# Optimization experiments

Measured on AMD Instinct MI355X. Metric: run time of the kernel, lower is better.

## Reference

```python
import jax, jax.numpy as jnp
import numpy as np

B, S, D, H, L = 4, 2048, 256, 4, 2
DK = D // H
V, T = 32000, 1000


def setup_inputs() -> dict:
    key = jax.random.key(0)
    ks = jax.random.split(key, 20)
    sc = 0.02
    event_emb = jax.random.normal(ks[0], (V, D), jnp.float32) * sc
    event_emb = event_emb.at[0].set(0.0)  # padding_idx=0
    time_emb = jax.random.normal(ks[1], (T, D), jnp.float32) * sc
    inp = {
        "x": jax.random.randint(ks[2], (B, S), 0, V, jnp.int32),
        "time_deltas": jax.random.randint(ks[3], (B, S), 0, T, jnp.int32),
        "mask": jax.random.randint(ks[4], (B, S), 0, 2, jnp.int32),
        "event_emb": event_emb,
        "time_emb": time_emb,
        "Wq": jax.random.normal(ks[5], (L, D, D), jnp.float32) * sc,
        "bq": jnp.zeros((L, D), jnp.float32),
        "Wk": jax.random.normal(ks[6], (L, D, D), jnp.float32) * sc,
        "bk": jnp.zeros((L, D), jnp.float32),
        "Wv": jax.random.normal(ks[7], (L, D, D), jnp.float32) * sc,
        "bv": jnp.zeros((L, D), jnp.float32),
        "time_proj": jax.random.normal(ks[8], (L, T, H), jnp.float32) * sc,
        "Wo": jax.random.normal(ks[9], (L, D, D), jnp.float32) * sc,
        "bo": jnp.zeros((L, D), jnp.float32),
        "ln_g": jnp.ones((L, D), jnp.float32),
        "ln_b": jnp.zeros((L, D), jnp.float32),
        "Wc1": jax.random.normal(ks[10], (D, D // 2), jnp.float32) * sc,
        "bc1": jnp.zeros((D // 2,), jnp.float32),
        "Wc2": jax.random.normal(ks[11], (D // 2, 1), jnp.float32) * sc,
        "bc2": jnp.zeros((1,), jnp.float32),
    }
    return inp


def _layernorm(h, g, b, eps=1e-5):
    mu = jnp.mean(h, -1, keepdims=True)
    var = jnp.mean(jnp.square(h - mu), -1, keepdims=True)
    return (h - mu) * jax.lax.rsqrt(var + eps) * g + b


def _attn(h, t_bins, mask, Wq, bq, Wk, bk, Wv, bv, tp, Wo, bo):
    b, s, d = h.shape
    q = (h @ Wq + bq).reshape(b, s, H, DK)
    k = (h @ Wk + bk).reshape(b, s, H, DK)
    v = (h @ Wv + bv).reshape(b, s, H, DK)
    scores = jnp.einsum("bqhd,bkhd->bhqk", q, k) / np.sqrt(DK).astype(np.float32)
    time_bias = tp[t_bins]  # [b,s,H] -> bias per key position
    scores = scores + jnp.transpose(time_bias, (0, 2, 1))[:, :, None, :]
    scores = jnp.where(mask[:, None, None, :] == 0, -1e9, scores)
    attn = jax.nn.softmax(scores, axis=-1)
    ctx = jnp.einsum("bhqk,bkhd->bqhd", attn, v).reshape(b, s, d)
    return ctx @ Wo + bo


def reference(x, time_deltas, mask, event_emb, time_emb, Wq, bq, Wk, bk, Wv, bv,
              time_proj, Wo, bo, ln_g, ln_b, Wc1, bc1, Wc2, bc2):
    t_bins = jnp.clip(time_deltas, 0, T - 1)
    h = event_emb[x] + time_emb[t_bins]
    for l in range(L):
        h = _attn(h, t_bins, mask, Wq[l], bq[l], Wk[l], bk[l], Wv[l], bv[l],
                  time_proj[l], Wo[l], bo[l])
        h = _layernorm(h, ln_g[l], ln_b[l])
    last = h[:, -1, :]
    hid = jax.nn.relu(last @ Wc1 + bc1)
    return jax.nn.sigmoid(hid @ Wc2 + bc2)
```

## Files before the change

### kernel.cpp

```cpp
#include <hip/hip_runtime.h>
#include <math.h>

namespace {

constexpr int NB = 4, NS = 2048, ND = 256, NH = 4, NDK = 64, NL = 2, NT = 1000;
constexpr float L2E = 1.44269504089f;
constexpr float QSCALE = 0.125f * L2E;

typedef short bfx8 __attribute__((ext_vector_type(8)));
typedef float f32x4 __attribute__((ext_vector_type(4)));

static __device__ __forceinline__ short f2bf(float f) {
  union { float f; unsigned u; } v; v.f = f;
  unsigned u = v.u;
  unsigned r = (u + 0x7fffu + ((u >> 16) & 1u)) >> 16;
  return (short)r;
}
static __device__ __forceinline__ float bf2f(short s) {
  union { float f; unsigned u; } v; v.u = ((unsigned)(unsigned short)s) << 16;
  return v.f;
}
static __device__ __forceinline__ float exp2_hw(float x) {
  float r;
  asm("v_exp_f32 %0, %1" : "=v"(r) : "v"(x));
  return r;
}
static __device__ __forceinline__ unsigned cvt_pk_bf16(float lo, float hi) {
  unsigned d;
  asm("v_cvt_pk_bf16_f32 %0, %1, %2" : "=v"(d) : "v"(lo), "v"(hi));
  return d;
}

__global__ __launch_bounds__(256) void k_packw(const float* __restrict__ Wq,
                                               const float* __restrict__ Wk,
                                               const float* __restrict__ Wv,
                                               const float* __restrict__ Wo,
                                               const float* __restrict__ bq,
                                               const float* __restrict__ bk,
                                               const float* __restrict__ bv,
                                               short* __restrict__ wqkvT,
                                               short* __restrict__ woT,
                                               float* __restrict__ bqkv) {
  __shared__ float t[64][65];
  int z = blockIdx.z, l = z >> 2, mat = z & 3;
  const float* src;
  short* dst;
  float scale = 1.f;
  if (mat == 0)      { src = Wq + (size_t)l * 65536; dst = wqkvT + (size_t)l * 768 * 256; scale = QSCALE; }
  else if (mat == 1) { src = Wk + (size_t)l * 65536; dst = wqkvT + (size_t)l * 768 * 256 + 256 * 256; }
  else if (mat == 2) { src = Wv + (size_t)l * 65536; dst = wqkvT + (size_t)l * 768 * 256 + 512 * 256; }
  else               { src = Wo + (size_t)l * 65536; dst = woT + (size_t)l * 65536; }
  int k0 = blockIdx.x * 64, n0 = blockIdx.y * 64;
  int c = threadIdx.x & 63, r4 = threadIdx.x >> 6;
  #pragma unroll
  for (int rr = 0; rr < 64; rr += 4) t[rr + r4][c] = src[(size_t)(k0 + rr + r4) * 256 + n0 + c];
  __syncthreads();
  #pragma unroll
  for (int rr = 0; rr < 64; rr += 4) {
    int n = rr + r4;
    dst[(size_t)(n0 + n) * 256 + k0 + c] = f2bf(t[c][n] * scale);
  }
  if (mat == 0 && blockIdx.x == 0 && blockIdx.y == 0) {
    for (int cc = threadIdx.x; cc < 768; cc += 256) {
      float v = cc < 256 ? bq[l * 256 + cc] * QSCALE
                         : (cc < 512 ? bk[l * 256 + cc - 256] : bv[l * 256 + cc - 512]);
      bqkv[l * 768 + cc] = v;
    }
  }
}

__global__ __launch_bounds__(256) void k_embed(const int* __restrict__ x,
                                               const int* __restrict__ td,
                                               const float* __restrict__ ee,
                                               const float* __restrict__ te,
                                               float* __restrict__ h,
                                               short* __restrict__ hb) {
  int lane = threadIdx.x & 63, r4 = threadIdx.x >> 6;
  int row = blockIdx.x * 4 + r4;
  int xi = x[row];
  int tb = td[row];
  tb = tb < 0 ? 0 : (tb >= NT ? NT - 1 : tb);
  float4 e = ((const float4*)&ee[(size_t)xi * ND])[lane];
  float4 tv = ((const float4*)&te[(size_t)tb * ND])[lane];
  float4 v;
  v.x = e.x + tv.x; v.y = e.y + tv.y; v.z = e.z + tv.z; v.w = e.w + tv.w;
  ((float4*)&h[(size_t)row * ND])[lane] = v;
  short4 ob; ob.x = f2bf(v.x); ob.y = f2bf(v.y); ob.z = f2bf(v.z); ob.w = f2bf(v.w);
  ((short4*)&hb[(size_t)row * ND])[lane] = ob;
}

template <int OUT_BF16>
__global__ __launch_bounds__(256) void k_gemm(const short* __restrict__ A,
                                              const short* __restrict__ BT,
                                              const float* __restrict__ bias,
                                              void* __restrict__ C, int ldc,
                                              int mb_mul, int mb_add, int n_base) {
  constexpr int LP = 76;
  __shared__ short at[64][LP];
  __shared__ short bt[128][LP];
  int tid = threadIdx.x;
  int w = tid >> 6, lane = tid & 63, ln15 = lane & 15, g = lane >> 4;
  int m0 = (blockIdx.x * mb_mul + mb_add) * 64;
  int n0 = n_base + blockIdx.y * 128;
  int srow = tid >> 2, scol = (tid & 3) * 16;
  int brow = tid >> 1, bcol = (tid & 1) * 32;

  f32x4 acc[8];
  #pragma unroll
  for (int nt = 0; nt < 8; ++nt) acc[nt] = (f32x4){0.f, 0.f, 0.f, 0.f};

  bfx8 a0, a1, b0, b1, b2, b3;
  auto LOAD = [&](int kk0) {
    const short* as = &A[(size_t)(m0 + srow) * 256 + kk0 + scol];
    a0 = *(const bfx8*)as; a1 = *(const bfx8*)(as + 8);
    const short* bs = &BT[(size_t)(n0 + brow) * 256 + kk0 + bcol];
    b0 = *(const bfx8*)bs; b1 = *(const bfx8*)(bs + 8);
    b2 = *(const bfx8*)(bs + 16); b3 = *(const bfx8*)(bs + 24);
  };
  LOAD(0);
  for (int kk0 = 0; kk0 < 256; kk0 += 64) {
    __syncthreads();
    *(bfx8*)&at[srow][scol] = a0; *(bfx8*)&at[srow][scol + 8] = a1;
    *(bfx8*)&bt[brow][bcol] = b0; *(bfx8*)&bt[brow][bcol + 8] = b1;
    *(bfx8*)&bt[brow][bcol + 16] = b2; *(bfx8*)&bt[brow][bcol + 24] = b3;
    __syncthreads();
    if (kk0 + 64 < 256) LOAD(kk0 + 64);
    #pragma unroll
    for (int ks = 0; ks < 2; ++ks) {
      bfx8 af = *(const bfx8*)&at[w * 16 + ln15][ks * 32 + g * 8];
      #pragma unroll
      for (int nt = 0; nt < 8; ++nt) {
        bfx8 bf = *(const bfx8*)&bt[nt * 16 + ln15][ks * 32 + g * 8];
        acc[nt] = __builtin_amdgcn_mfma_f32_16x16x32_bf16(af, bf, acc[nt], 0, 0, 0);
      }
    }
  }

  #pragma unroll
  for (int nt = 0; nt < 8; ++nt) {
    int col = n0 + nt * 16 + ln15;
    float bb = bias[col];
    #pragma unroll
    for (int r = 0; r < 4; ++r) {
      int row = m0 + w * 16 + g * 4 + r;
      float val = acc[nt][r] + bb;
      if (OUT_BF16) ((short*)C)[(size_t)row * ldc + col] = f2bf(val);
      else          ((float*)C)[(size_t)row * ldc + col] = val;
    }
  }
}

__global__ __launch_bounds__(256) void k_pmerge(const short* __restrict__ partO,
                                                const float* __restrict__ partML,
                                                const short* __restrict__ BT,
                                                const float* __restrict__ bias,
                                                float* __restrict__ C) {
  constexpr int LP = 76;
  constexpr int NC = 4;
  __shared__ short at[64][LP];
  __shared__ short bt[128][LP];
  int tid = threadIdx.x;
  int w = tid >> 6, lane = tid & 63, ln15 = lane & 15, g = lane >> 4;
  int m0 = blockIdx.x * 64;
  int n0 = blockIdx.y * 128;
  int srow = tid >> 2, scol = (tid & 3) * 16;
  int brow = tid >> 1, bcol = (tid & 1) * 32;

  int grow = m0 + srow;
  int b = grow >> 11, s = grow & 2047;

  f32x4 acc[8];
  #pragma unroll
  for (int nt = 0; nt < 8; ++nt) acc[nt] = (f32x4){0.f, 0.f, 0.f, 0.f};

  bfx8 a0, a1, b0_, b1_, b2_, b3_;
  auto LOAD = [&](int kk0) {
    int hh2 = kk0 >> 6;
    size_t rbase = (size_t)(b * NH + hh2) * NS + s;
    float2 ml[NC];
    float M = -1e30f;
    #pragma unroll
    for (int c = 0; c < NC; ++c) {
      ml[c] = *(const float2*)&partML[(rbase + (size_t)c * 16 * NS) * 2];
      M = fmaxf(M, ml[c].x);
    }
    float wgt[NC], L = 0.f;
    #pragma unroll
    for (int c = 0; c < NC; ++c) { wgt[c] = exp2_hw(ml[c].x - M); L += ml[c].y * wgt[c]; }
    float inv = 1.f / L;
    float av[16];
    #pragma unroll
    for (int i = 0; i < 16; ++i) av[i] = 0.f;
    #pragma unroll
    for (int c = 0; c < NC; ++c) {
      float wc = wgt[c] * inv;
      size_t row = rbase + (size_t)c * 16 * NS;
      union { int4 v; short sh[8]; } ua, ub;
      ua.v = *(const int4*)&partO[row * 64 + scol];
      ub.v = *(const int4*)&partO[row * 64 + scol + 8];
      #pragma unroll
      for (int i = 0; i < 8; ++i) {
        av[i]     = fmaf(bf2f(ua.sh[i]), wc, av[i]);
        av[8 + i] = fmaf(bf2f(ub.sh[i]), wc, av[8 + i]);
      }
    }
    union { bfx8 v; short sh[8]; } pa, pb;
    #pragma unroll
    for (int i = 0; i < 8; ++i) { pa.sh[i] = f2bf(av[i]); pb.sh[i] = f2bf(av[8 + i]); }
    a0 = pa.v; a1 = pb.v;
    const short* bs = &BT[(size_t)(n0 + brow) * 256 + kk0 + bcol];
    b0_ = *(const bfx8*)bs; b1_ = *(const bfx8*)(bs + 8);
    b2_ = *(const bfx8*)(bs + 16); b3_ = *(const bfx8*)(bs + 24);
  };
  LOAD(0);
  for (int kk0 = 0; kk0 < 256; kk0 += 64) {
    __syncthreads();
    *(bfx8*)&at[srow][scol] = a0; *(bfx8*)&at[srow][scol + 8] = a1;
    *(bfx8*)&bt[brow][bcol] = b0_; *(bfx8*)&bt[brow][bcol + 8] = b1_;
    *(bfx8*)&bt[brow][bcol + 16] = b2_; *(bfx8*)&bt[brow][bcol + 24] = b3_;
    __syncthreads();
    if (kk0 + 64 < 256) LOAD(kk0 + 64);
    #pragma unroll
    for (int ks = 0; ks < 2; ++ks) {
      bfx8 af = *(const bfx8*)&at[w * 16 + ln15][ks * 32 + g * 8];
      #pragma unroll
      for (int nt = 0; nt < 8; ++nt) {
        bfx8 bf = *(const bfx8*)&bt[nt * 16 + ln15][ks * 32 + g * 8];
        acc[nt] = __builtin_amdgcn_mfma_f32_16x16x32_bf16(af, bf, acc[nt], 0, 0, 0);
      }
    }
  }

  #pragma unroll
  for (int nt = 0; nt < 8; ++nt) {
    int col = n0 + nt * 16 + ln15;
    float bb = bias[col];
    #pragma unroll
    for (int r = 0; r < 4; ++r) {
      int row = m0 + w * 16 + g * 4 + r;
      C[(size_t)row * 256 + col] = acc[nt][r] + bb;
    }
  }
}

__global__ __launch_bounds__(256) void k_frag(const short* __restrict__ qkv,
                                              const int* __restrict__ td,
                                              const int* __restrict__ mask,
                                              const float* __restrict__ tp,
                                              short* __restrict__ vT,
                                              float* __restrict__ sbias_g) {
  __shared__ short vl[64][72];
  int tile = blockIdx.x, hh = blockIdx.y, b = blockIdx.z;
  int t = threadIdx.x;
  int k0 = tile * 64;
  {
    int key = t >> 2, dg = (t & 3) * 16;
    const short* vsrc = &qkv[(size_t)(b * NS + k0 + key) * 768 + 512 + hh * NDK + dg];
    bfx8 v0 = *(const bfx8*)vsrc, v1 = *(const bfx8*)(vsrc + 8);
    *(bfx8*)&vl[key][dg] = v0;
    *(bfx8*)&vl[key][dg + 8] = v1;
  }
  if (t < 64) {
    int kk = k0 + t;
    int tb = td[b * NS + kk];
    tb = tb < 0 ? 0 : (tb >= NT ? NT - 1 : tb);
    sbias_g[(size_t)(b * NH + hh) * NS + kk] = mask[b * NS + kk] ? tp[tb * NH + hh] * L2E : -1e9f;
  }
  __syncthreads();
  int dim = t >> 2, c0 = (t & 3) * 16;
  short outv[16];
  #pragma unroll
  for (int j = 0; j < 16; ++j) {
    int c = c0 + j;
    int kk = ((c >> 5) << 5) | (((c >> 2) & 1) << 4) | (((c >> 3) & 3) << 2) | (c & 3);
    outv[j] = vl[kk][dim];
  }
  short* dst = &vT[(((size_t)(b * NH + hh) * 32 + tile) * 64 + dim) * 64 + c0];
  *(int4*)dst = *(const int4*)outv;
  *(int4*)(dst + 8) = *(const int4*)(outv + 8);
}

__global__ __launch_bounds__(512, 4) void k_attn(const short* __restrict__ qkv,
                                                 const short* __restrict__ vT,
                                                 const float* __restrict__ sbias_g,
                                                 short* __restrict__ ctx,
                                                 short* __restrict__ partO,
                                                 float* __restrict__ partML,
                                                 int q_base, int qcount, int nchunk) {
  constexpr int LPK = 76;
  constexpr int LPV = 76;
  __shared__ short kt[2][64][LPK];
  __shared__ short vt[2][64][LPV];
  __shared__ float sbias[2][64];
  __shared__ float shML[128];

  int tid = threadIdx.x;
  int w = tid >> 6, lane = tid & 63, ln15 = lane & 15, g = lane >> 4;
  int half = w >> 2, wsub = w & 3;
  int t = tid & 255;
  int b = blockIdx.z, hh = blockIdx.y;
  int qtile = blockIdx.x / nchunk;
  int chunk = blockIdx.x - qtile * nchunk;
  int niter = NS / (128 * nchunk);
  int tbase = chunk * (NS / 64 / nchunk);
  int q0 = q_base + qtile * 64;
  int qw0 = q0 + wsub * 16;

  bfx8 aq[2];
  #pragma unroll
  for (int ks = 0; ks < 2; ++ks)
    aq[ks] = *(const bfx8*)&qkv[(size_t)(b * NS + qw0 + ln15) * 768 + hh * NDK + ks * 32 + g * 8];

  f32x4 o[4];
  #pragma unroll
  for (int dt = 0; dt < 4; ++dt) o[dt] = (f32x4){0.f, 0.f, 0.f, 0.f};
  float m = -1e30f, lsum = 0.f;

  int srow = t >> 2, scg = (t & 3) * 16;

  bfx8 kr0, kr1, vr0, vr1;
  float br = 0.f;
  auto loadset = [&](int it) {
    int tt = tbase + half * niter + it;
    int k0 = tt * 64;
    const short* ksrc = &qkv[(size_t)(b * NS + k0 + srow) * 768 + 256 + hh * NDK + scg];
    kr0 = *(const bfx8*)ksrc; kr1 = *(const bfx8*)(ksrc + 8);
    const short* vsrc = &vT[(((size_t)(b * NH + hh) * 32 + tt) * 64 + srow) * 64 + scg];
    vr0 = *(const bfx8*)vsrc; vr1 = *(const bfx8*)(vsrc + 8);
    if (t < 64) br = sbias_g[(size_t)(b * NH + hh) * NS + k0 + t];
  };

  auto compute = [&]() {
    f32x4 c[4];
    __builtin_amdgcn_s_setprio(1);
    #pragma unroll
    for (int nt = 0; nt < 4; ++nt) {
      c[nt] = (f32x4){0.f, 0.f, 0.f, 0.f};
      #pragma unroll
      for (int ks = 0; ks < 2; ++ks) {
        bfx8 kf = *(const bfx8*)&kt[half][nt * 16 + ln15][ks * 32 + g * 8];
        c[nt] = __builtin_amdgcn_mfma_f32_16x16x32_bf16(kf, aq[ks], c[nt], 0, 0, 0);
      }
    }
    __builtin_amdgcn_s_setprio(0);
    #pragma unroll
    for (int nt = 0; nt < 4; ++nt) {
      float4 bb = *(const float4*)&sbias[half][nt * 16 + g * 4];
      c[nt][0] += bb.x; c[nt][1] += bb.y; c[nt][2] += bb.z; c[nt][3] += bb.w;
    }
    float rm = c[0][0];
    #pragma unroll
    for (int nt = 0; nt < 4; ++nt)
      #pragma unroll
      for (int r = 0; r < 4; ++r) rm = fmaxf(rm, c[nt][r]);
    rm = fmaxf(rm, __shfl_xor(rm, 16, 64));
    rm = fmaxf(rm, __shfl_xor(rm, 32, 64));
    if (__any(rm > m + 10.f)) {
      float nm = fmaxf(m, rm);
      float scl = exp2_hw(m - nm);
      m = nm;
      lsum *= scl;
      #pragma unroll
      for (int dt = 0; dt < 4; ++dt)
        #pragma unroll
        for (int r = 0; r < 4; ++r) o[dt][r] *= scl;
    }
    unsigned pb[2][4];
    float ts = 0.f;
    #pragma unroll
    for (int nt = 0; nt < 4; ++nt) {
      float e0 = exp2_hw(c[nt][0] - m), e1 = exp2_hw(c[nt][1] - m);
      float e2 = exp2_hw(c[nt][2] - m), e3 = exp2_hw(c[nt][3] - m);
      ts += (e0 + e1) + (e2 + e3);
      pb[nt >> 1][(nt & 1) * 2]     = cvt_pk_bf16(e0, e1);
      pb[nt >> 1][(nt & 1) * 2 + 1] = cvt_pk_bf16(e2, e3);
    }
    lsum += ts;
    __builtin_amdgcn_s_setprio(1);
    #pragma unroll
    for (int ks = 0; ks < 2; ++ks) {
      union { unsigned u[4]; bfx8 v; } pf;
      pf.u[0] = pb[ks][0]; pf.u[1] = pb[ks][1]; pf.u[2] = pb[ks][2]; pf.u[3] = pb[ks][3];
      #pragma unroll
      for (int dt = 0; dt < 4; ++dt) {
        bfx8 vf = *(const bfx8*)&vt[half][dt * 16 + ln15][ks * 32 + g * 8];
        o[dt] = __builtin_amdgcn_mfma_f32_16x16x32_bf16(vf, pf.v, o[dt], 0, 0, 0);
      }
    }
    __builtin_amdgcn_s_setprio(0);
  };

  loadset(0);
  for (int it = 0; it < niter; ++it) {
    __syncthreads();
    *(bfx8*)&kt[half][srow][scg] = kr0;
    *(bfx8*)&kt[half][srow][scg + 8] = kr1;
    *(bfx8*)&vt[half][srow][scg] = vr0;
    *(bfx8*)&vt[half][srow][scg + 8] = vr1;
    if (t < 64) sbias[half][t] = br;
    __syncthreads();
    if (it + 1 < niter) loadset(it + 1);
    compute();
  }

  lsum += __shfl_xor(lsum, 16, 64);
  lsum += __shfl_xor(lsum, 32, 64);

  float* shO = (float*)&kt[0][0][0];
  __syncthreads();
  int q = wsub * 16 + ln15;
  if (half == 1) {
    #pragma unroll
    for (int dt = 0; dt < 4; ++dt) {
      float4 st; st.x = o[dt][0]; st.y = o[dt][1]; st.z = o[dt][2]; st.w = o[dt][3];
      *(float4*)&shO[q * 68 + dt * 16 + g * 4] = st;
    }
    if (g == 0) { shML[q * 2] = m; shML[q * 2 + 1] = lsum; }
  }
  __syncthreads();
  if (half == 0) {
    float m2 = shML[q * 2], l2 = shML[q * 2 + 1];
    float M = fmaxf(m, m2);
    float fa = exp2_hw(m - M), fb = exp2_hw(m2 - M);
    if (nchunk == 1) {
      float inv = 1.f / (lsum * fa + l2 * fb);
      fa *= inv; fb *= inv;
      #pragma unroll
      for (int dt = 0; dt < 4; ++dt) {
        float4 sh = *(const float4*)&shO[q * 68 + dt * 16 + g * 4];
        float v0 = o[dt][0] * fa + sh.x * fb;
        float v1 = o[dt][1] * fa + sh.y * fb;
        float v2 = o[dt][2] * fa + sh.z * fb;
        float v3 = o[dt][3] * fa + sh.w * fb;
        int2 pk; pk.x = (int)cvt_pk_bf16(v0, v1); pk.y = (int)cvt_pk_bf16(v2, v3);
        *(int2*)&ctx[(size_t)(b * NS + q0 + q) * ND + hh * NDK + dt * 16 + g * 4] = pk;
      }
    } else {
      float L = lsum * fa + l2 * fb;
      size_t rowi = (size_t)(chunk * 16 + b * NH + hh) * qcount + qtile * 64 + q;
      #pragma unroll
      for (int dt = 0; dt < 4; ++dt) {
        float4 sh = *(const float4*)&shO[q * 68 + dt * 16 + g * 4];
        float v0 = o[dt][0] * fa + sh.x * fb;
        float v1 = o[dt][1] * fa + sh.y * fb;
        float v2 = o[dt][2] * fa + sh.z * fb;
        float v3 = o[dt][3] * fa + sh.w * fb;
        int2 pk; pk.x = (int)cvt_pk_bf16(v0, v1); pk.y = (int)cvt_pk_bf16(v2, v3);
        *(int2*)&partO[rowi * 64 + dt * 16 + g * 4] = pk;
      }
      if (g == 0) { partML[rowi * 2] = M; partML[rowi * 2 + 1] = L; }
    }
  }
}

__global__ __launch_bounds__(256) void k_amerge(const short* __restrict__ partO,
                                                const float* __restrict__ partML,
                                                short* __restrict__ ctx,
                                                int q_base, int qcount, int nchunk) {
  int b = blockIdx.z, hh = blockIdx.y;
  int qi = blockIdx.x * 64 + (threadIdx.x >> 2);
  int d0 = (threadIdx.x & 3) * 16;
  int bh = b * NH + hh;
  float M = -1e30f;
  for (int c = 0; c < nchunk; ++c)
    M = fmaxf(M, partML[((size_t)(c * 16 + bh) * qcount + qi) * 2]);
  float L = 0.f;
  float acc[16];
  #pragma unroll
  for (int i = 0; i < 16; ++i) acc[i] = 0.f;
  for (int c = 0; c < nchunk; ++c) {
    size_t row = (size_t)(c * 16 + bh) * qcount + qi;
    float mc = partML[row * 2];
    float lc = partML[row * 2 + 1];
    float s = exp2_hw(mc - M);
    L += lc * s;
    union { int4 v; short sh[8]; } u0, u1;
    u0.v = *(const int4*)&partO[row * 64 + d0];
    u1.v = *(const int4*)&partO[row * 64 + d0 + 8];
    #pragma unroll
    for (int i = 0; i < 8; ++i) {
      acc[i]     += bf2f(u0.sh[i]) * s;
      acc[8 + i] += bf2f(u1.sh[i]) * s;
    }
  }
  float inv = 1.f / L;
  short res[16];
  #pragma unroll
  for (int i = 0; i < 16; ++i) res[i] = f2bf(acc[i] * inv);
  short* dst = &ctx[(size_t)(b * NS + q_base + qi) * ND + hh * NDK + d0];
  *(int4*)dst = *(const int4*)res;
  *(int4*)(dst + 8) = *(const int4*)(res + 8);
}

__global__ __launch_bounds__(256) void k_ln(float* __restrict__ h,
                                            short* __restrict__ hb,
                                            const float* __restrict__ g_,
                                            const float* __restrict__ b_, int q_base) {
  int lane = threadIdx.x & 63, r4 = threadIdx.x >> 6;
  size_t row = (size_t)blockIdx.y * NS + q_base + blockIdx.x * 4 + r4;
  float4 v = ((const float4*)&h[row * ND])[lane];
  float s = v.x + v.y + v.z + v.w;
  #pragma unroll
  for (int off = 1; off < 64; off <<= 1) s += __shfl_xor(s, off, 64);
  float mu = s * (1.f / ND);
  float dx = v.x - mu, dy = v.y - mu, dz = v.z - mu, dw = v.w - mu;
  float q = dx * dx + dy * dy + dz * dz + dw * dw;
  #pragma unroll
  for (int off = 1; off < 64; off <<= 1) q += __shfl_xor(q, off, 64);
  float rr = rsqrtf(q * (1.f / ND) + 1e-5f);
  float4 gg = ((const float4*)g_)[lane];
  float4 bb = ((const float4*)b_)[lane];
  float4 o;
  o.x = dx * rr * gg.x + bb.x;
  o.y = dy * rr * gg.y + bb.y;
  o.z = dz * rr * gg.z + bb.z;
  o.w = dw * rr * gg.w + bb.w;
  ((float4*)&h[row * ND])[lane] = o;
  short4 ob; ob.x = f2bf(o.x); ob.y = f2bf(o.y); ob.z = f2bf(o.z); ob.w = f2bf(o.w);
  ((short4*)&hb[row * ND])[lane] = ob;
}

__global__ __launch_bounds__(128) void k_head(const float* __restrict__ h,
                                              const float* __restrict__ Wc1,
                                              const float* __restrict__ bc1,
                                              const float* __restrict__ Wc2,
                                              const float* __restrict__ bc2,
                                              float* __restrict__ out) {
  __shared__ float red[128];
  int j = threadIdx.x;
  int b = blockIdx.x;
  const float* last = &h[(size_t)(b * NS + NS - 1) * ND];
  float acc = bc1[j];
  for (int d = 0; d < ND; ++d) acc = fmaf(last[d], Wc1[d * 128 + j], acc);
  acc = fmaxf(acc, 0.f);
  red[j] = acc * Wc2[j];
  __syncthreads();
  for (int off = 64; off > 0; off >>= 1) {
    if (j < off) red[j] += red[j + off];
    __syncthreads();
  }
  if (j == 0) out[b] = 1.f / (1.f + __expf(-(red[0] + bc2[0])));
}

}

extern "C" void kernel_launch(void* const* d_in, const int* in_sizes, int n_in,
                              void* d_out, int out_size, void* d_ws, size_t ws_size,
                              hipStream_t stream) {
  const int* x = (const int*)d_in[0];
  const int* td = (const int*)d_in[1];
  const int* mask = (const int*)d_in[2];
  const float* ee = (const float*)d_in[3];
  const float* te = (const float*)d_in[4];
  const float* Wq = (const float*)d_in[5];
  const float* bq = (const float*)d_in[6];
  const float* Wk = (const float*)d_in[7];
  const float* bk = (const float*)d_in[8];
  const float* Wv = (const float*)d_in[9];
  const float* bv = (const float*)d_in[10];
  const float* tp = (const float*)d_in[11];
  const float* Wo = (const float*)d_in[12];
  const float* bo = (const float*)d_in[13];
  const float* lng = (const float*)d_in[14];
  const float* lnb = (const float*)d_in[15];
  const float* Wc1 = (const float*)d_in[16];
  const float* bc1 = (const float*)d_in[17];
  const float* Wc2 = (const float*)d_in[18];
  const float* bc2 = (const float*)d_in[19];
  float* out = (float*)d_out;

  char* ws = (char*)d_ws;
  const size_t M = (size_t)NB * NS;
  short* qkv     = (short*)(ws);
  float* h       = (float*)(ws + (12 << 20));
  short* hb      = (short*)(ws + (20 << 20));
  short* vT      = (short*)(ws + (24 << 20));
  float* sbias_g = (float*)(ws + (28 << 20));
  short* wqkvT   = (short*)(ws + (28 << 20) + (128 << 10));
  short* woT     = (short*)(ws + (28 << 20) + (896 << 10));
  float* bqkv    = (float*)(ws + (28 << 20) + (1152 << 10));
  short* partO   = (short*)(ws + (30 << 20));
  float* partML  = (float*)(ws + (47 << 20));
  short* ctx1    = vT;

  k_packw<<<dim3(4, 4, 8), 256, 0, stream>>>(Wq, Wk, Wv, Wo, bq, bk, bv, wqkvT, woT, bqkv);
  k_embed<<<NB * NS / 4, 256, 0, stream>>>(x, td, ee, te, h, hb);

  for (int l = 0; l < NL; ++l) {
    const short* wqkvTl = wqkvT + (size_t)l * 768 * 256;
    const short* woTl = woT + (size_t)l * 65536;
    const float* bqkvl = bqkv + (size_t)l * 768;
    const float* bol = bo + (size_t)l * ND;
    const float* tpl = tp + (size_t)l * NT * NH;
    const float* lngl = lng + (size_t)l * ND;
    const float* lnbl = lnb + (size_t)l * ND;
    const bool last = (l == NL - 1);

    if (!last) {
      k_gemm<1><<<dim3(M / 64, 6), 256, 0, stream>>>(hb, wqkvTl, bqkvl, qkv, 768, 1, 0, 0);
    } else {
      k_gemm<1><<<dim3(M / 64, 4), 256, 0, stream>>>(hb, wqkvTl, bqkvl, qkv, 768, 1, 0, 256);
      k_gemm<1><<<dim3(NB, 2), 256, 0, stream>>>(hb, wqkvTl, bqkvl, qkv, 768, 32, 31, 0);
    }

    k_frag<<<dim3(32, NH, NB), 256, 0, stream>>>(qkv, td, mask, tpl, vT, sbias_g);

    if (!last) {
      k_attn<<<dim3((NS / 64) * 4, NH, NB), 512, 0, stream>>>(qkv, vT, sbias_g, partO,
                                                              partO, partML, 0, NS, 4);
      k_pmerge<<<dim3(M / 64, 2), 256, 0, stream>>>(partO, partML, woTl, bol, h);
      k_ln<<<dim3(NS / 4, NB), 256, 0, stream>>>(h, hb, lngl, lnbl, 0);
    } else {
      k_attn<<<dim3(16, NH, NB), 512, 0, stream>>>(qkv, vT, sbias_g, ctx1,
                                                   partO, partML, NS - 64, 64, 16);
      k_amerge<<<dim3(1, NH, NB), 256, 0, stream>>>(partO, partML, ctx1, NS - 64, 64, 16);
      k_gemm<0><<<dim3(NB, 2), 256, 0, stream>>>(ctx1, woTl, bol, h, 256, 32, 31, 0);
      k_ln<<<dim3(1, NB), 256, 0, stream>>>(h, hb, lngl, lnbl, NS - 4);
    }
  }

  k_head<<<NB, 128, 0, stream>>>(h, Wc1, bc1, Wc2, bc2, out);
}
```

Before: 131.0 us.

## Read K/V fragments directly from global memory and halve attention key-chunk split

The attention kernel no longer stages K, V and the bias through double-buffered shared memory with barriers. Each wave now loads its MFMA operands straight from global memory (served by L1/L2), and shared memory is kept only for the final half-merge. The non-last layer also drops from 4 to 2 key chunks, with the partial-merge chunk count NC changed to match, so there are fewer partials to merge. The aim is to remove LDS traffic and per-iteration syncs, at the cost of uncoalesced strided global reads with no prefetch and fewer blocks in flight.

```diff
diff --git a/kernel.cpp b/kernel.cpp
--- a/kernel.cpp
+++ b/kernel.cpp
@@ -156,7 +156,7 @@
                                                 const float* __restrict__ bias,
                                                 float* __restrict__ C) {
   constexpr int LP = 76;
-  constexpr int NC = 4;
+  constexpr int NC = 2;
   __shared__ short at[64][LP];
   __shared__ short bt[128][LP];
   int tid = threadIdx.x;
@@ -287,18 +287,14 @@
                                                  short* __restrict__ partO,
                                                  float* __restrict__ partML,
                                                  int q_base, int qcount, int nchunk) {
-  constexpr int LPK = 76;
-  constexpr int LPV = 76;
-  __shared__ short kt[2][64][LPK];
-  __shared__ short vt[2][64][LPV];
-  __shared__ float sbias[2][64];
+  __shared__ float shO[64 * 68];
   __shared__ float shML[128];
 
   int tid = threadIdx.x;
   int w = tid >> 6, lane = tid & 63, ln15 = lane & 15, g = lane >> 4;
   int half = w >> 2, wsub = w & 3;
-  int t = tid & 255;
   int b = blockIdx.z, hh = blockIdx.y;
+  int bh = b * NH + hh;
   int qtile = blockIdx.x / nchunk;
   int chunk = blockIdx.x - qtile * nchunk;
   int niter = NS / (128 * nchunk);
@@ -316,21 +312,13 @@
   for (int dt = 0; dt < 4; ++dt) o[dt] = (f32x4){0.f, 0.f, 0.f, 0.f};
   float m = -1e30f, lsum = 0.f;
 
-  int srow = t >> 2, scg = (t & 3) * 16;
-
-  bfx8 kr0, kr1, vr0, vr1;
-  float br = 0.f;
-  auto loadset = [&](int it) {
+  for (int it = 0; it < niter; ++it) {
     int tt = tbase + half * niter + it;
-    int k0 = tt * 64;
-    const short* ksrc = &qkv[(size_t)(b * NS + k0 + srow) * 768 + 256 + hh * NDK + scg];
-    kr0 = *(const bfx8*)ksrc; kr1 = *(const bfx8*)(ksrc + 8);
-    const short* vsrc = &vT[(((size_t)(b * NH + hh) * 32 + tt) * 64 + srow) * 64 + scg];
-    vr0 = *(const bfx8*)vsrc; vr1 = *(const bfx8*)(vsrc + 8);
-    if (t < 64) br = sbias_g[(size_t)(b * NH + hh) * NS + k0 + t];
-  };
-
-  auto compute = [&]() {
+    int k0t = tt * 64;
+    const short* kp = &qkv[(size_t)(b * NS + k0t) * 768 + 256 + hh * NDK];
+    const short* vp = &vT[(size_t)(bh * 32 + tt) * 64 * 64];
+    const float* bp = &sbias_g[(size_t)bh * NS + k0t];
+
     f32x4 c[4];
     __builtin_amdgcn_s_setprio(1);
     #pragma unroll
@@ -338,14 +326,14 @@
       c[nt] = (f32x4){0.f, 0.f, 0.f, 0.f};
       #pragma unroll
       for (int ks = 0; ks < 2; ++ks) {
-        bfx8 kf = *(const bfx8*)&kt[half][nt * 16 + ln15][ks * 32 + g * 8];
+        bfx8 kf = *(const bfx8*)&kp[(size_t)(nt * 16 + ln15) * 768 + ks * 32 + g * 8];
         c[nt] = __builtin_amdgcn_mfma_f32_16x16x32_bf16(kf, aq[ks], c[nt], 0, 0, 0);
       }
     }
     __builtin_amdgcn_s_setprio(0);
     #pragma unroll
     for (int nt = 0; nt < 4; ++nt) {
-      float4 bb = *(const float4*)&sbias[half][nt * 16 + g * 4];
+      float4 bb = *(const float4*)&bp[nt * 16 + g * 4];
       c[nt][0] += bb.x; c[nt][1] += bb.y; c[nt][2] += bb.z; c[nt][3] += bb.w;
     }
     float rm = c[0][0];
@@ -383,30 +371,16 @@
       pf.u[0] = pb[ks][0]; pf.u[1] = pb[ks][1]; pf.u[2] = pb[ks][2]; pf.u[3] = pb[ks][3];
       #pragma unroll
       for (int dt = 0; dt < 4; ++dt) {
-        bfx8 vf = *(const bfx8*)&vt[half][dt * 16 + ln15][ks * 32 + g * 8];
+        bfx8 vf = *(const bfx8*)&vp[(size_t)(dt * 16 + ln15) * 64 + ks * 32 + g * 8];
         o[dt] = __builtin_amdgcn_mfma_f32_16x16x32_bf16(vf, pf.v, o[dt], 0, 0, 0);
       }
     }
     __builtin_amdgcn_s_setprio(0);
-  };
-
-  loadset(0);
-  for (int it = 0; it < niter; ++it) {
-    __syncthreads();
-    *(bfx8*)&kt[half][srow][scg] = kr0;
-    *(bfx8*)&kt[half][srow][scg + 8] = kr1;
-    *(bfx8*)&vt[half][srow][scg] = vr0;
-    *(bfx8*)&vt[half][srow][scg + 8] = vr1;
-    if (t < 64) sbias[half][t] = br;
-    __syncthreads();
-    if (it + 1 < niter) loadset(it + 1);
-    compute();
   }
 
   lsum += __shfl_xor(lsum, 16, 64);
   lsum += __shfl_xor(lsum, 32, 64);
 
-  float* shO = (float*)&kt[0][0][0];
   __syncthreads();
   int q = wsub * 16 + ln15;
   if (half == 1) {
@@ -437,7 +411,7 @@
       }
     } else {
       float L = lsum * fa + l2 * fb;
-      size_t rowi = (size_t)(chunk * 16 + b * NH + hh) * qcount + qtile * 64 + q;
+      size_t rowi = (size_t)(chunk * 16 + bh) * qcount + qtile * 64 + q;
       #pragma unroll
       for (int dt = 0; dt < 4; ++dt) {
         float4 sh = *(const float4*)&shO[q * 68 + dt * 16 + g * 4];
@@ -606,8 +580,8 @@
     k_frag<<<dim3(32, NH, NB), 256, 0, stream>>>(qkv, td, mask, tpl, vT, sbias_g);
 
     if (!last) {
-      k_attn<<<dim3((NS / 64) * 4, NH, NB), 512, 0, stream>>>(qkv, vT, sbias_g, partO,
-                                                              partO, partML, 0, NS, 4);
+      k_attn<<<dim3((NS / 64) * 2, NH, NB), 512, 0, stream>>>(qkv, vT, sbias_g, partO,
+                                                              partO, partML, 0, NS, 2);
       k_pmerge<<<dim3(M / 64, 2), 256, 0, stream>>>(partO, partML, woTl, bol, h);
       k_ln<<<dim3(NS / 4, NB), 256, 0, stream>>>(h, hb, lngl, lnbl, 0);
     } else {
```

Result: slower. 218.4 us (+66.8%).
